# Performance work log

Measured on AMD Instinct MI355X. Metric: run time of the kernel, lower is better.

The kernel has to match this reference:

```python
import jax, jax.numpy as jnp
import numpy as np

B, N, H, HEADS, L, V, T = 4, 256, 256, 4, 128, 256, 100
FF = 4 * H

def _ln(x, g, b, eps=1e-5):
    m = jnp.mean(x, -1, keepdims=True)
    v = jnp.mean((x - m) ** 2, -1, keepdims=True)
    return (x - m) / jnp.sqrt(v + eps) * g + b

def _mha(h, w_qkv, b_qkv, w_o, b_o):
    b, n, hd = h.shape
    d = hd // HEADS
    q, k, v = jnp.split(h @ w_qkv + b_qkv, 3, axis=-1)
    q = q.reshape(b, n, HEADS, d)
    k = k.reshape(b, n, HEADS, d)
    v = v.reshape(b, n, HEADS, d)
    s = jnp.einsum('bihd,bjhd->bhij', q, k) / jnp.sqrt(jnp.float32(d))
    a = jax.nn.softmax(s, axis=-1)
    o = jnp.einsum('bhij,bjhd->bihd', a, v).reshape(b, n, hd)
    return o @ w_o + b_o

def _edge_logits(h, w1, b1, w2, b2):
    # concat([h_i, h_j], -1) @ w1 == h_i @ w1[:H] + h_j @ w1[H:]  (avoids (B,N,N,2H) materialization)
    hi = h @ w1[:H]
    hj = h @ w1[H:]
    pre = hi[:, :, None, :] + hj[:, None, :, :] + b1  # (B,N,N,H)
    return (jax.nn.gelu(pre, approximate=False) @ w2 + b2)[..., 0]

def _gnn_block(x, nbr, qw, qb, kw, kb, vw, vb, sw, sb, l1g, l1b, f1w, f1b, f2w, f2b, l2g, l2b):
    # TransformerConv (PyG, concat=True, root_weight=True) as dense masked attention over in-neighbors.
    b, n, hd = x.shape
    d = hd // HEADS
    q = (x @ qw + qb).reshape(b, n, HEADS, d)
    k = (x @ kw + kb).reshape(b, n, HEADS, d)
    v = (x @ vw + vb).reshape(b, n, HEADS, d)
    s = jnp.einsum('bihd,bjhd->bhij', q, k) / jnp.sqrt(jnp.float32(d))
    m = nbr[:, None, :, :]  # (B,1,N,N); nbr[b,i,j]=True iff edge j->i
    a = jax.nn.softmax(jnp.where(m, s, -1e30), axis=-1) * m  # no-neighbor rows aggregate to 0
    agg = jnp.einsum('bhij,bjhd->bihd', a, v).reshape(b, n, hd)
    x = _ln(x + agg + x @ sw + sb, l1g, l1b)
    ffn = jax.nn.gelu(x @ f1w + f1b, approximate=False) @ f2w + f2b
    return _ln(x + ffn, l2g, l2b)

def _forward(noisy_tokens, t, z, lp1_w, lp1_b, lp2_w, lp2_b, tok_emb, time_tab, time_w, time_b, pos_tab, enc_qkv_w, enc_qkv_b, enc_o_w, enc_o_b, enc_ln1_g, enc_ln1_b, enc_f1_w, enc_f1_b, enc_f2_w, enc_f2_b, enc_ln2_g, enc_ln2_b, gq_w, gq_b, gk_w, gk_b, gv_w, gv_b, gs_w, gs_b, g_ln1_g, g_ln1_b, g_f1_w, g_f1_b, g_f2_w, g_f2_b, g_ln2_g, g_ln2_b, nh1_w, nh1_b, nh2_w, nh2_b, eh1_w, eh1_b, eh2_w, eh2_b, sh1_w, sh1_b, sh2_w, sh2_b):
    lat = jax.nn.relu(z @ lp1_w + lp1_b) @ lp2_w + lp2_b  # (B,H)
    time_e = jax.nn.gelu(time_tab[t] @ time_w + time_b, approximate=False)  # (B,H)
    h = tok_emb[noisy_tokens] + time_e[:, None, :] + pos_tab[None, :, :] + lat[:, None, :]
    for l in range(2):  # post-norm TransformerEncoderLayer, relu FFN
        h = _ln(h + _mha(h, enc_qkv_w[l], enc_qkv_b[l], enc_o_w[l], enc_o_b[l]), enc_ln1_g[l], enc_ln1_b[l])
        h = _ln(h + jax.nn.relu(h @ enc_f1_w[l] + enc_f1_b[l]) @ enc_f2_w[l] + enc_f2_b[l], enc_ln2_g[l], enc_ln2_b[l])
    el0 = _edge_logits(h, eh1_w, eh1_b, eh2_w, eh2_b)
    nbr = jnp.swapaxes(jax.nn.sigmoid(el0) > 0.3, 1, 2)  # transpose: adj[j,i] -> in-neighbors of i
    x = h
    for l in range(4):
        x = _gnn_block(x, nbr, gq_w[l], gq_b[l], gk_w[l], gk_b[l], gv_w[l], gv_b[l], gs_w[l], gs_b[l], g_ln1_g[l], g_ln1_b[l], g_f1_w[l], g_f1_b[l], g_f2_w[l], g_f2_b[l], g_ln2_g[l], g_ln2_b[l])
    node_logits = jax.nn.gelu(x @ nh1_w + nh1_b, approximate=False) @ nh2_w + nh2_b
    edge_logits = _edge_logits(x, eh1_w, eh1_b, eh2_w, eh2_b)
    size_logits = jax.nn.relu(lat @ sh1_w + sh1_b) @ sh2_w + sh2_b
    return node_logits, edge_logits, size_logits

def setup_inputs():
    key = jax.random.key(0)
    ks = iter(jax.random.split(key, 70))
    def p(shape):
        return jax.random.normal(next(ks), shape, dtype=jnp.float32) * 0.02
    return {
        'z': jax.random.normal(next(ks), (B, L), dtype=jnp.float32),
        'noisy_tokens': jax.random.randint(next(ks), (B, N), 0, V),
        't': jax.random.randint(next(ks), (B,), 0, T),
        'lp1_w': p((L, H)), 'lp1_b': p((H,)), 'lp2_w': p((H, H)), 'lp2_b': p((H,)),
        'tok_emb': p((V, H)), 'time_tab': p((T, H)), 'time_w': p((H, H)), 'time_b': p((H,)),
        'pos_tab': p((N, H)),
        'enc_qkv_w': p((2, H, 3 * H)), 'enc_qkv_b': p((2, 3 * H)),
        'enc_o_w': p((2, H, H)), 'enc_o_b': p((2, H)),
        'enc_ln1_g': jnp.ones((2, H)), 'enc_ln1_b': jnp.zeros((2, H)),
        'enc_f1_w': p((2, H, FF)), 'enc_f1_b': p((2, FF)),
        'enc_f2_w': p((2, FF, H)), 'enc_f2_b': p((2, H)),
        'enc_ln2_g': jnp.ones((2, H)), 'enc_ln2_b': jnp.zeros((2, H)),
        'gq_w': p((4, H, H)), 'gq_b': p((4, H)),
        'gk_w': p((4, H, H)), 'gk_b': p((4, H)),
        'gv_w': p((4, H, H)), 'gv_b': p((4, H)),
        'gs_w': p((4, H, H)), 'gs_b': p((4, H)),
        'g_ln1_g': jnp.ones((4, H)), 'g_ln1_b': jnp.zeros((4, H)),
        'g_f1_w': p((4, H, FF)), 'g_f1_b': p((4, FF)),
        'g_f2_w': p((4, FF, H)), 'g_f2_b': p((4, H)),
        'g_ln2_g': jnp.ones((4, H)), 'g_ln2_b': jnp.zeros((4, H)),
        'nh1_w': p((H, H)), 'nh1_b': p((H,)),
        'nh2_w': p((H, V)), 'nh2_b': p((V,)),
        'eh1_w': p((2 * H, H)), 'eh1_b': p((H,)),
        'eh2_w': p((H, 1)), 'eh2_b': p((1,)),
        'sh1_w': p((H, H // 2)), 'sh1_b': p((H // 2,)),
        'sh2_w': p((H // 2, N)), 'sh2_b': p((N,)),
    }

def reference(z, noisy_tokens, t, lp1_w, lp1_b, lp2_w, lp2_b, tok_emb, time_tab, time_w, time_b, pos_tab, enc_qkv_w, enc_qkv_b, enc_o_w, enc_o_b, enc_ln1_g, enc_ln1_b, enc_f1_w, enc_f1_b, enc_f2_w, enc_f2_b, enc_ln2_g, enc_ln2_b, gq_w, gq_b, gk_w, gk_b, gv_w, gv_b, gs_w, gs_b, g_ln1_g, g_ln1_b, g_f1_w, g_f1_b, g_f2_w, g_f2_b, g_ln2_g, g_ln2_b, nh1_w, nh1_b, nh2_w, nh2_b, eh1_w, eh1_b, eh2_w, eh2_b, sh1_w, sh1_b, sh2_w, sh2_b):
    return _forward(noisy_tokens, t, z, lp1_w, lp1_b, lp2_w, lp2_b, tok_emb, time_tab, time_w, time_b, pos_tab, enc_qkv_w, enc_qkv_b, enc_o_w, enc_o_b, enc_ln1_g, enc_ln1_b, enc_f1_w, enc_f1_b, enc_f2_w, enc_f2_b, enc_ln2_g, enc_ln2_b, gq_w, gq_b, gk_w, gk_b, gv_w, gv_b, gs_w, gs_b, g_ln1_g, g_ln1_b, g_f1_w, g_f1_b, g_f2_w, g_f2_b, g_ln2_g, g_ln2_b, nh1_w, nh1_b, nh2_w, nh2_b, eh1_w, eh1_b, eh2_w, eh2_b, sh1_w, sh1_b, sh2_w, sh2_b)
```

## Files before the change

kernel.cpp:

```cpp
#include <hip/hip_runtime.h>
#include <math.h>


typedef __attribute__((ext_vector_type(8))) short bf16x8;
typedef __attribute__((ext_vector_type(4))) float f32x4;

__device__ __forceinline__ unsigned short f2b(float f) {
    unsigned u = __float_as_uint(f);
    u += 0x7FFFu + ((u >> 16) & 1u);
    return (unsigned short)(u >> 16);
}
__device__ __forceinline__ unsigned pack2(float a, float b) {
    return (unsigned)f2b(a) | ((unsigned)f2b(b) << 16);
}
__device__ __forceinline__ bf16x8 as_frag(uint4 v) {
    union { uint4 u; bf16x8 f; } x; x.u = v; return x.f;
}
__device__ __forceinline__ bf16x8 ld_frag_f32(const float* p) {
    const float4 v0 = *(const float4*)p;
    const float4 v1 = *(const float4*)(p + 4);
    union { unsigned u[4]; bf16x8 f; } x;
    x.u[0] = pack2(v0.x, v0.y); x.u[1] = pack2(v0.z, v0.w);
    x.u[2] = pack2(v1.x, v1.y); x.u[3] = pack2(v1.z, v1.w);
    return x.f;
}

__device__ __forceinline__ float gelu_f(float x) {
    const float y  = 0.70710678118654752f * x;
    const float ay = fabsf(y);
    const float t  = __builtin_amdgcn_rcpf(fmaf(0.3275911f, ay, 1.0f));
    float S = fmaf(t, 1.061405429f, -1.453152027f);
    S = fmaf(t, S, 1.421413741f);
    S = fmaf(t, S, -0.284496736f);
    S = fmaf(t, S, 0.254829592f);
    S = S * t;
    const float e = __expf(-ay * ay);
    const float E = fmaf(-S, e, 1.0f);
    return 0.5f * x * (1.0f + copysignf(E, y));
}

struct PrepEnt { const float* src; unsigned dstOff; int K; int N; unsigned tstart; };
struct PrepTab { int n; PrepEnt e[36]; };

__global__ __launch_bounds__(256) void k_prep(PrepTab tab, unsigned short* __restrict__ wt)
{
    const int bx = blockIdx.x;
    int ei = 0;
    for (int i = 0; i < tab.n; ++i) if (tab.e[i].tstart <= (unsigned)bx) ei = i;
    const PrepEnt E = tab.e[ei];
    const int tIdx = bx - E.tstart;
    const int ntn = E.N >> 6;
    const int kt = tIdx / ntn, nt = tIdx % ntn;
    const int tid = threadIdx.x;
    __shared__ unsigned Tl[64][36];
    {
        const int r = tid >> 2, c = (tid & 3) * 16;
        const float* s = E.src + (size_t)(kt * 64 + r) * E.N + nt * 64 + c;
        unsigned o[8];
        #pragma unroll
        for (int q = 0; q < 4; ++q) {
            const float4 v = *(const float4*)(s + q * 4);
            o[q * 2 + 0] = pack2(v.x, v.y);
            o[q * 2 + 1] = pack2(v.z, v.w);
        }
        *(uint4*)&Tl[r][c / 2 + 0] = make_uint4(o[0], o[1], o[2], o[3]);
        *(uint4*)&Tl[r][c / 2 + 4] = make_uint4(o[4], o[5], o[6], o[7]);
    }
    __syncthreads();
    {
        const int rn = tid >> 2, ck = (tid & 3) * 16;
        const int sh = (rn & 1) * 16, hw = rn >> 1;
        unsigned o[8];
        #pragma unroll
        for (int s = 0; s < 8; ++s) {
            const unsigned lo = (Tl[ck + 2 * s][hw] >> sh) & 0xFFFFu;
            const unsigned hi = (Tl[ck + 2 * s + 1][hw] >> sh) & 0xFFFFu;
            o[s] = lo | (hi << 16);
        }
        unsigned short* d = wt + E.dstOff + (size_t)(nt * 64 + rn) * E.K + kt * 64 + ck;
        *(uint4*)(d + 0) = make_uint4(o[0], o[1], o[2], o[3]);
        *(uint4*)(d + 8) = make_uint4(o[4], o[5], o[6], o[7]);
    }
}


__device__ __forceinline__ void gd64_body(
    const float* __restrict__ A, const unsigned short* __restrict__ Wt,
    const float* __restrict__ bias, float* __restrict__ C,
    int K, int ldc, int act, int m0, int n0)
{
    const int tid = threadIdx.x;
    const int l = tid & 63, wid = tid >> 6;
    const int wm = wid & 1, wn = wid >> 1, lr = l & 15, lg = l >> 4;
    const float* a0 = A + (size_t)(m0 + wm * 32 + lr) * K + lg * 8;
    const float* a1 = a0 + (size_t)16 * K;
    const unsigned short* b0 = Wt + (size_t)(n0 + wn * 32 + lr) * K + lg * 8;
    const unsigned short* b1 = b0 + (size_t)16 * K;
    f32x4 acc00 = {0.f,0.f,0.f,0.f}, acc01 = acc00, acc10 = acc00, acc11 = acc00;
    #pragma unroll 2
    for (int k0 = 0; k0 < K; k0 += 32) {
        const bf16x8 fa0 = ld_frag_f32(a0 + k0);
        const bf16x8 fa1 = ld_frag_f32(a1 + k0);
        const bf16x8 fb0 = as_frag(*(const uint4*)(b0 + k0));
        const bf16x8 fb1 = as_frag(*(const uint4*)(b1 + k0));
        acc00 = __builtin_amdgcn_mfma_f32_16x16x32_bf16(fa0, fb0, acc00, 0, 0, 0);
        acc01 = __builtin_amdgcn_mfma_f32_16x16x32_bf16(fa0, fb1, acc01, 0, 0, 0);
        acc10 = __builtin_amdgcn_mfma_f32_16x16x32_bf16(fa1, fb0, acc10, 0, 0, 0);
        acc11 = __builtin_amdgcn_mfma_f32_16x16x32_bf16(fa1, fb1, acc11, 0, 0, 0);
    }
    const int cb0 = n0 + wn * 32 + lr, cb1 = cb0 + 16;
    const float bv0 = bias ? bias[cb0] : 0.f;
    const float bv1 = bias ? bias[cb1] : 0.f;
    #pragma unroll
    for (int r = 0; r < 4; ++r) {
        const int row0 = m0 + wm * 32 + lg * 4 + r;
        const int row1 = row0 + 16;
        float v00 = acc00[r] + bv0, v01 = acc01[r] + bv1;
        float v10 = acc10[r] + bv0, v11 = acc11[r] + bv1;
        if (act == 1) {
            v00 = fmaxf(v00, 0.f); v01 = fmaxf(v01, 0.f);
            v10 = fmaxf(v10, 0.f); v11 = fmaxf(v11, 0.f);
        } else if (act == 2) {
            v00 = gelu_f(v00); v01 = gelu_f(v01);
            v10 = gelu_f(v10); v11 = gelu_f(v11);
        }
        C[(size_t)row0 * ldc + cb0] = v00;
        C[(size_t)row0 * ldc + cb1] = v01;
        C[(size_t)row1 * ldc + cb0] = v10;
        C[(size_t)row1 * ldc + cb1] = v11;
    }
}

__global__ __launch_bounds__(256) void k_gd64(
    const float* __restrict__ A, const unsigned short* __restrict__ Wt,
    const float* __restrict__ bias, float* __restrict__ C, int K, int ldc, int act)
{
    gd64_body(A, Wt, bias, C, K, ldc, act, blockIdx.y * 64, blockIdx.x * 64);
}

__device__ __forceinline__ void gd32_body(
    const float* __restrict__ A, const unsigned short* __restrict__ Wt,
    const float* __restrict__ bias, float* __restrict__ C,
    int K, int ldc, int act, int m0, int n0)
{
    const int tid = threadIdx.x;
    const int l = tid & 63, wid = tid >> 6;
    const int qm = wid & 1, qn = wid >> 1, lr = l & 15, lg = l >> 4;
    const float* ap = A + (size_t)(m0 + qm * 16 + lr) * K + lg * 8;
    const unsigned short* bp = Wt + (size_t)(n0 + qn * 16 + lr) * K + lg * 8;
    f32x4 acc = {0.f,0.f,0.f,0.f};
    #pragma unroll 4
    for (int k0 = 0; k0 < K; k0 += 32) {
        const bf16x8 fa = ld_frag_f32(ap + k0);
        const bf16x8 fb = as_frag(*(const uint4*)(bp + k0));
        acc = __builtin_amdgcn_mfma_f32_16x16x32_bf16(fa, fb, acc, 0, 0, 0);
    }
    const int cc = n0 + qn * 16 + lr;
    const float bv = bias ? bias[cc] : 0.f;
    #pragma unroll
    for (int r = 0; r < 4; ++r) {
        const int row = m0 + qm * 16 + lg * 4 + r;
        float v = acc[r] + bv;
        if (act == 1) v = fmaxf(v, 0.f); else if (act == 2) v = gelu_f(v);
        C[(size_t)row * ldc + cc] = v;
    }
}

__global__ __launch_bounds__(256) void k_gd32(
    const float* __restrict__ A, const unsigned short* __restrict__ Wt,
    const float* __restrict__ bias, float* __restrict__ C, int K, int ldc, int act)
{
    gd32_body(A, Wt, bias, C, K, ldc, act, blockIdx.y * 32, blockIdx.x * 32);
}

struct MW4 { const unsigned short* wt[4]; const float* b[4]; };
__global__ __launch_bounds__(256) void k_gd32_4(
    const float* __restrict__ A, MW4 p, float* __restrict__ C)
{
    const int z = blockIdx.z;
    gd32_body(A, p.wt[z], p.b[z], C + z * 256, 256, 1024, 0,
              blockIdx.y * 32, blockIdx.x * 32);
}

__global__ __launch_bounds__(256) void k_mv(
    const float* __restrict__ A, const int* __restrict__ aidx, int K,
    const float* __restrict__ W, const float* __restrict__ bias,
    float* __restrict__ out, int N, int act)
{
    const int r = blockIdx.x, c0 = blockIdx.y * 64;
    const int c = threadIdx.x & 63, ks = threadIdx.x >> 6;
    const float* arow = A + (size_t)(aidx ? aidx[r] : r) * K;
    float s = 0.f;
    for (int k = ks; k < K; k += 4) s += arow[k] * W[(size_t)k * N + c0 + c];
    __shared__ float red[4][64];
    red[ks][c] = s;
    __syncthreads();
    if (ks == 0) {
        float v = red[0][c] + red[1][c] + red[2][c] + red[3][c] + (bias ? bias[c0 + c] : 0.f);
        if (act == 1) v = fmaxf(v, 0.f); else if (act == 2) v = gelu_f(v);
        out[(size_t)r * N + c0 + c] = v;
    }
}

__global__ __launch_bounds__(256) void k_embed(
    const int* __restrict__ tok, const float* __restrict__ tok_emb,
    const float* __restrict__ pos, const float* __restrict__ lat,
    const float* __restrict__ te, float* __restrict__ h)
{
    const int r = blockIdx.x, c = threadIdx.x;
    const int b = r >> 8, n = r & 255;
    h[(size_t)r * 256 + c] = tok_emb[(size_t)tok[r] * 256 + c] + te[b * 256 + c]
                           + pos[n * 256 + c] + lat[b * 256 + c];
}

__global__ __launch_bounds__(256) void k_attn2(
    const float* __restrict__ qkv, int ld, int qo, int ko, int vo,
    const unsigned char* __restrict__ mask, float* __restrict__ out)
{
    const int blk = blockIdx.x;
    const int ig = blk & 15, hh = (blk >> 4) & 3, b = blk >> 6;
    const int i0 = ig * 16;
    const int t = threadIdx.x;
    __shared__ float Qs[16][68];
    __shared__ float Ts[64][68];
    __shared__ float Ss[16][260];

    {
        const int r = t >> 4, c = (t & 15) * 4;
        *(float4*)&Qs[r][c] = *(const float4*)&qkv[(size_t)(b * 256 + i0 + r) * ld + qo + hh * 64 + c];
    }
    const int i = t >> 4, tx = t & 15;

    for (int jt = 0; jt < 4; ++jt) {
        __syncthreads();
        {
            const int jr = t >> 2, cs = (t & 3) * 16;
            const float* src = &qkv[(size_t)(b * 256 + jt * 64 + jr) * ld + ko + hh * 64 + cs];
            *(float4*)&Ts[jr][cs + 0]  = *(const float4*)(src + 0);
            *(float4*)&Ts[jr][cs + 4]  = *(const float4*)(src + 4);
            *(float4*)&Ts[jr][cs + 8]  = *(const float4*)(src + 8);
            *(float4*)&Ts[jr][cs + 12] = *(const float4*)(src + 12);
        }
        __syncthreads();
        float s0 = 0.f, s1 = 0.f, s2 = 0.f, s3 = 0.f;
        #pragma unroll 8
        for (int d = 0; d < 64; ++d) {
            const float qd = Qs[i][d];
            s0 += qd * Ts[tx][d];
            s1 += qd * Ts[tx + 16][d];
            s2 += qd * Ts[tx + 32][d];
            s3 += qd * Ts[tx + 48][d];
        }
        Ss[i][jt * 64 + tx]      = s0;
        Ss[i][jt * 64 + tx + 16] = s1;
        Ss[i][jt * 64 + tx + 32] = s2;
        Ss[i][jt * 64 + tx + 48] = s3;
    }

    {
        const unsigned char* mrow = mask ? &mask[(size_t)(b * 256 + i0 + i) * 256] : nullptr;
        float sv[16]; bool okv[16];
        float m = -3.0e38f;
        #pragma unroll
        for (int k = 0; k < 16; ++k) {
            const int j = tx + 16 * k;
            const float s = Ss[i][j] * 0.125f;
            const bool ok = mrow ? (mrow[j] != 0) : true;
            sv[k] = s; okv[k] = ok;
            if (ok) m = fmaxf(m, s);
        }
        #pragma unroll
        for (int w = 1; w < 16; w <<= 1) m = fmaxf(m, __shfl_xor(m, w, 64));
        float ev[16]; float sum = 0.f;
        #pragma unroll
        for (int k = 0; k < 16; ++k) {
            ev[k] = okv[k] ? __expf(sv[k] - m) : 0.f;
            sum += ev[k];
        }
        #pragma unroll
        for (int w = 1; w < 16; w <<= 1) sum += __shfl_xor(sum, w, 64);
        const float inv = (sum > 0.f) ? 1.f / sum : 0.f;
        #pragma unroll
        for (int k = 0; k < 16; ++k) Ss[i][tx + 16 * k] = ev[k] * inv;
    }

    const int d4 = tx * 4;
    float4 o = {0.f, 0.f, 0.f, 0.f};
    for (int jt = 0; jt < 4; ++jt) {
        __syncthreads();
        {
            const int jr = t >> 2, cs = (t & 3) * 16;
            const float* src = &qkv[(size_t)(b * 256 + jt * 64 + jr) * ld + vo + hh * 64 + cs];
            *(float4*)&Ts[jr][cs + 0]  = *(const float4*)(src + 0);
            *(float4*)&Ts[jr][cs + 4]  = *(const float4*)(src + 4);
            *(float4*)&Ts[jr][cs + 8]  = *(const float4*)(src + 8);
            *(float4*)&Ts[jr][cs + 12] = *(const float4*)(src + 12);
        }
        __syncthreads();
        #pragma unroll 8
        for (int j = 0; j < 64; ++j) {
            const float p = Ss[i][jt * 64 + j];
            const float4 v4 = *(const float4*)&Ts[j][d4];
            o.x += p * v4.x; o.y += p * v4.y; o.z += p * v4.z; o.w += p * v4.w;
        }
    }
    *(float4*)&out[(size_t)(b * 256 + i0 + i) * 256 + hh * 64 + d4] = o;
}

__global__ __launch_bounds__(256) void k_ln2(
    const float* __restrict__ a, const float* __restrict__ bb, int ldb,
    const float* __restrict__ cc, int ldc,
    const float* __restrict__ g, const float* __restrict__ beta, float* __restrict__ out)
{
    const int r = blockIdx.x * 4 + (threadIdx.x >> 6);
    const int c4 = (threadIdx.x & 63) * 4;
    float4 v = *(const float4*)&a[(size_t)r * 256 + c4];
    if (bb) {
        const float4 u = *(const float4*)&bb[(size_t)r * ldb + c4];
        v.x += u.x; v.y += u.y; v.z += u.z; v.w += u.w;
    }
    if (cc) {
        const float4 u = *(const float4*)&cc[(size_t)r * ldc + c4];
        v.x += u.x; v.y += u.y; v.z += u.z; v.w += u.w;
    }
    float s = v.x + v.y + v.z + v.w;
    float q = v.x * v.x + v.y * v.y + v.z * v.z + v.w * v.w;
    #pragma unroll
    for (int w = 1; w < 64; w <<= 1) {
        s += __shfl_xor(s, w, 64);
        q += __shfl_xor(q, w, 64);
    }
    const float mean = s * (1.0f / 256.0f);
    const float var  = q * (1.0f / 256.0f) - mean * mean;
    const float inv  = rsqrtf(var + 1e-5f);
    const float4 gg = *(const float4*)&g[c4];
    const float4 be = *(const float4*)&beta[c4];
    float4 o;
    o.x = (v.x - mean) * inv * gg.x + be.x;
    o.y = (v.y - mean) * inv * gg.y + be.y;
    o.z = (v.z - mean) * inv * gg.z + be.z;
    o.w = (v.w - mean) * inv * gg.w + be.w;
    *(float4*)&out[(size_t)r * 256 + c4] = o;
}

__global__ __launch_bounds__(256) void k_edge3(
    const float* __restrict__ hi, const float* __restrict__ hj,
    const float* __restrict__ w2, const float* __restrict__ b2,
    float* __restrict__ val_out, unsigned char* __restrict__ mask_out)
{
    const int jg = blockIdx.x, ig = blockIdx.y, b = blockIdx.z;
    const int t = threadIdx.x;
    __shared__ float his[16][268];
    __shared__ float hjs[16][268];
    __shared__ float w2s[256];
    {
        const int r = t >> 4, c = (t & 15) * 16;
        const float* s1 = &hi[(size_t)(b * 256 + ig * 16 + r) * 256 + c];
        const float* s2 = &hj[(size_t)(b * 256 + jg * 16 + r) * 256 + c];
        #pragma unroll
        for (int q = 0; q < 4; ++q) {
            *(float4*)&his[r][c + q * 4] = *(const float4*)(s1 + q * 4);
            *(float4*)&hjs[r][c + q * 4] = *(const float4*)(s2 + q * 4);
        }
        w2s[t] = w2[t];
    }
    __syncthreads();
    const int i = t >> 4, j = t & 15;
    float acc = 0.f;
    #pragma unroll 4
    for (int h4 = 0; h4 < 64; ++h4) {
        const float4 hv  = *(const float4*)&hjs[j][h4 * 4];
        const float4 hi4 = *(const float4*)&his[i][h4 * 4];
        const float4 w4  = *(const float4*)&w2s[h4 * 4];
        acc += gelu_f(hi4.x + hv.x) * w4.x;
        acc += gelu_f(hi4.y + hv.y) * w4.y;
        acc += gelu_f(hi4.z + hv.z) * w4.z;
        acc += gelu_f(hi4.w + hv.w) * w4.w;
    }
    const float v = acc + b2[0];
    if (val_out)  val_out[(size_t)b * 65536 + (ig * 16 + i) * 256 + jg * 16 + j] = v;
    if (mask_out) mask_out[(size_t)b * 65536 + (jg * 16 + j) * 256 + ig * 16 + i] =
                      (v > -0.84729786038720f) ? 1 : 0;
}

extern "C" void kernel_launch(void* const* d_in, const int* in_sizes, int n_in,
                              void* d_out, int out_size, void* d_ws, size_t ws_size,
                              hipStream_t stream) {
    const float* z     = (const float*)d_in[0];
    const int*   tok   = (const int*)d_in[1];
    const int*   tt    = (const int*)d_in[2];
    const float* lp1w  = (const float*)d_in[3];
    const float* lp1b  = (const float*)d_in[4];
    const float* lp2w  = (const float*)d_in[5];
    const float* lp2b  = (const float*)d_in[6];
    const float* temb  = (const float*)d_in[7];
    const float* ttab  = (const float*)d_in[8];
    const float* tw    = (const float*)d_in[9];
    const float* tb    = (const float*)d_in[10];
    const float* pos   = (const float*)d_in[11];
    const float* qkvw  = (const float*)d_in[12];
    const float* qkvb  = (const float*)d_in[13];
    const float* ow    = (const float*)d_in[14];
    const float* ob    = (const float*)d_in[15];
    const float* ln1g  = (const float*)d_in[16];
    const float* ln1b  = (const float*)d_in[17];
    const float* f1w   = (const float*)d_in[18];
    const float* f1b   = (const float*)d_in[19];
    const float* f2w   = (const float*)d_in[20];
    const float* f2b   = (const float*)d_in[21];
    const float* ln2g  = (const float*)d_in[22];
    const float* ln2b  = (const float*)d_in[23];
    const float* gqw   = (const float*)d_in[24];
    const float* gqb   = (const float*)d_in[25];
    const float* gkw   = (const float*)d_in[26];
    const float* gkb   = (const float*)d_in[27];
    const float* gvw   = (const float*)d_in[28];
    const float* gvb   = (const float*)d_in[29];
    const float* gsw   = (const float*)d_in[30];
    const float* gsb   = (const float*)d_in[31];
    const float* gl1g  = (const float*)d_in[32];
    const float* gl1b  = (const float*)d_in[33];
    const float* gf1w  = (const float*)d_in[34];
    const float* gf1b  = (const float*)d_in[35];
    const float* gf2w  = (const float*)d_in[36];
    const float* gf2b  = (const float*)d_in[37];
    const float* gl2g  = (const float*)d_in[38];
    const float* gl2b  = (const float*)d_in[39];
    const float* nh1w  = (const float*)d_in[40];
    const float* nh1b  = (const float*)d_in[41];
    const float* nh2w  = (const float*)d_in[42];
    const float* nh2b  = (const float*)d_in[43];
    const float* eh1w  = (const float*)d_in[44];
    const float* eh1b  = (const float*)d_in[45];
    const float* eh2w  = (const float*)d_in[46];
    const float* eh2b  = (const float*)d_in[47];
    const float* sh1w  = (const float*)d_in[48];
    const float* sh1b  = (const float*)d_in[49];
    const float* sh2w  = (const float*)d_in[50];
    const float* sh2b  = (const float*)d_in[51];

    float* W = (float*)d_ws;
    float* Hh  = W + 0;
    float* QK  = W + 262144;
    float* AO  = W + 1310720;
    float* T1  = W + 1572864;
    float* HI  = W + 1835008;
    float* HJ  = W + 2097152;
    float* LAT = W + 2359296;
    float* TE  = W + 2360320;
    float* A1  = W + 2361344;
    float* SH  = W + 2362368;
    unsigned char* MASK = (unsigned char*)(W + 2362880);
    unsigned short* wt  = (unsigned short*)(W + 2428416);

    float* out      = (float*)d_out;
    float* out_node = out;
    float* out_edge = out + 262144;
    float* out_sz   = out + 524288;

    PrepTab tab; int ne = 0; unsigned tiles = 0;
    auto add = [&](const float* src, int K, int N, unsigned off) {
        tab.e[ne].src = src; tab.e[ne].K = K; tab.e[ne].N = N;
        tab.e[ne].dstOff = off; tab.e[ne].tstart = tiles;
        tiles += (unsigned)((K >> 6) * (N >> 6)); ++ne;
    };
    for (int l = 0; l < 2; ++l) add(qkvw + (size_t)l * 196608, 256, 768,  0 + l * 196608);
    for (int l = 0; l < 2; ++l) add(ow   + (size_t)l * 65536,  256, 256,  393216 + l * 65536);
    for (int l = 0; l < 2; ++l) add(f1w  + (size_t)l * 262144, 256, 1024, 524288 + l * 262144);
    for (int l = 0; l < 2; ++l) add(f2w  + (size_t)l * 262144, 1024, 256, 1048576 + l * 262144);
    for (int l = 0; l < 4; ++l) add(gqw  + (size_t)l * 65536,  256, 256,  1572864 + l * 65536);
    for (int l = 0; l < 4; ++l) add(gkw  + (size_t)l * 65536,  256, 256,  1835008 + l * 65536);
    for (int l = 0; l < 4; ++l) add(gvw  + (size_t)l * 65536,  256, 256,  2097152 + l * 65536);
    for (int l = 0; l < 4; ++l) add(gsw  + (size_t)l * 65536,  256, 256,  2359296 + l * 65536);
    for (int l = 0; l < 4; ++l) add(gf1w + (size_t)l * 262144, 256, 1024, 2621440 + l * 262144);
    for (int l = 0; l < 4; ++l) add(gf2w + (size_t)l * 262144, 1024, 256, 3670016 + l * 262144);
    add(nh1w, 256, 256, 4718592);
    add(nh2w, 256, 256, 4784128);
    add(eh1w,         256, 256, 4849664);
    add(eh1w + 65536, 256, 256, 4915200);
    tab.n = ne;
    k_prep<<<tiles, 256, 0, stream>>>(tab, wt);

    auto g64 = [&](const float* Aa, size_t wtoff, const float* bias, float* Cc,
                   int N, int K, int ldc, int act) {
        k_gd64<<<dim3(N / 64, 16), 256, 0, stream>>>(Aa, wt + wtoff, bias, Cc, K, ldc, act);
    };
    auto g32 = [&](const float* Aa, size_t wtoff, const float* bias, float* Cc,
                   int K, int ldc, int act) {
        k_gd32<<<dim3(8, 32), 256, 0, stream>>>(Aa, wt + wtoff, bias, Cc, K, ldc, act);
    };

    k_mv<<<dim3(4, 4), 256, 0, stream>>>(z,    nullptr, 128, lp1w, lp1b, A1,     256, 1);
    k_mv<<<dim3(4, 4), 256, 0, stream>>>(ttab, tt,      256, tw,   tb,   TE,     256, 2);
    k_mv<<<dim3(4, 4), 256, 0, stream>>>(A1,   nullptr, 256, lp2w, lp2b, LAT,    256, 0);
    k_mv<<<dim3(4, 2), 256, 0, stream>>>(LAT,  nullptr, 256, sh1w, sh1b, SH,     128, 1);
    k_mv<<<dim3(4, 4), 256, 0, stream>>>(SH,   nullptr, 128, sh2w, sh2b, out_sz, 256, 0);

    k_embed<<<1024, 256, 0, stream>>>(tok, temb, pos, LAT, TE, Hh);

    for (int l = 0; l < 2; ++l) {
        g64(Hh, (size_t)l * 196608, qkvb + l * 768, QK, 768, 256, 768, 0);
        k_attn2<<<256, 256, 0, stream>>>(QK, 768, 0, 256, 512, nullptr, AO);
        g32(AO, 393216 + (size_t)l * 65536, ob + l * 256, T1, 256, 256, 0);
        k_ln2<<<256, 256, 0, stream>>>(Hh, T1, 256, nullptr, 0, ln1g + l * 256, ln1b + l * 256, Hh);
        g64(Hh, 524288 + (size_t)l * 262144, f1b + l * 1024, QK, 1024, 256, 1024, 1);
        g32(QK, 1048576 + (size_t)l * 262144, f2b + l * 256, T1, 1024, 256, 0);
        k_ln2<<<256, 256, 0, stream>>>(Hh, T1, 256, nullptr, 0, ln2g + l * 256, ln2b + l * 256, Hh);
    }

    g32(Hh, 4849664, eh1b, HI, 256, 256, 0);
    g32(Hh, 4915200, nullptr, HJ, 256, 256, 0);
    k_edge3<<<dim3(16, 16, 4), 256, 0, stream>>>(HI, HJ, eh2w, eh2b, nullptr, MASK);

    for (int l = 0; l < 4; ++l) {
        MW4 p;
        p.wt[0] = wt + 1572864 + (size_t)l * 65536; p.b[0] = gqb + l * 256;
        p.wt[1] = wt + 1835008 + (size_t)l * 65536; p.b[1] = gkb + l * 256;
        p.wt[2] = wt + 2097152 + (size_t)l * 65536; p.b[2] = gvb + l * 256;
        p.wt[3] = wt + 2359296 + (size_t)l * 65536; p.b[3] = gsb + l * 256;
        k_gd32_4<<<dim3(8, 32, 4), 256, 0, stream>>>(Hh, p, QK);
        k_attn2<<<256, 256, 0, stream>>>(QK, 1024, 0, 256, 512, MASK, AO);
        k_ln2<<<256, 256, 0, stream>>>(Hh, AO, 256, QK + 768, 1024, gl1g + l * 256, gl1b + l * 256, Hh);
        g64(Hh, 2621440 + (size_t)l * 262144, gf1b + l * 1024, QK, 1024, 256, 1024, 2);
        g32(QK, 3670016 + (size_t)l * 262144, gf2b + l * 256, T1, 1024, 256, 0);
        k_ln2<<<256, 256, 0, stream>>>(Hh, T1, 256, nullptr, 0, gl2g + l * 256, gl2b + l * 256, Hh);
    }

    g32(Hh, 4718592, nh1b, T1, 256, 256, 2);
    g32(T1, 4784128, nh2b, out_node, 256, 256, 0);
    g32(Hh, 4849664, eh1b, HI, 256, 256, 0);
    g32(Hh, 4915200, nullptr, HJ, 256, 256, 0);
    k_edge3<<<dim3(16, 16, 4), 256, 0, stream>>>(HI, HJ, eh2w, eh2b, out_edge, nullptr);
}
```

Measured before the change: 750.0 us.

## Fuse prep, latent/time MLPs and embedding into one kernel; batch independent GEMMs

Folds weight prep, the small latent, time and size matvec chains and the embedding build into one combined launch, using extra blocks after the prep tiles. Independent GEMMs (HI/HJ, nh1/HI/HJ) are batched into multi-target launches. The final edge head and the node-head GEMM share one kernel. The 64x64 GEMM variant is replaced by the 32x32 one with larger grids. The aim is to cut launch count and tail idle time, at the cost of serial per-block matvecs and a 32-tile GEMM with less reuse per block.

```diff
diff --git a/kernel.cpp b/kernel.cpp
--- a/kernel.cpp
+++ b/kernel.cpp
@@ -42,100 +42,98 @@
 struct PrepEnt { const float* src; unsigned dstOff; int K; int N; unsigned tstart; };
 struct PrepTab { int n; PrepEnt e[36]; };
 
-__global__ __launch_bounds__(256) void k_prep(PrepTab tab, unsigned short* __restrict__ wt)
-{
+struct S0Args {
+    const float *z; const int *tok, *tt;
+    const float *lp1w,*lp1b,*lp2w,*lp2b,*ttab,*tw,*tb,*temb,*pos;
+    const float *sh1w,*sh1b,*sh2w,*sh2b;
+    float *Hh, *out_sz;
+};
+
+__global__ __launch_bounds__(256) void k_combo1(PrepTab tab, unsigned short* __restrict__ wt,
+                                                S0Args A)
+{
+    __shared__ unsigned Tl[64][36];
+    __shared__ float zS[256], a1S[256], latS[256], teS[256];
+    __shared__ int tokS[256];
     const int bx = blockIdx.x;
-    int ei = 0;
-    for (int i = 0; i < tab.n; ++i) if (tab.e[i].tstart <= (unsigned)bx) ei = i;
-    const PrepEnt E = tab.e[ei];
-    const int tIdx = bx - E.tstart;
-    const int ntn = E.N >> 6;
-    const int kt = tIdx / ntn, nt = tIdx % ntn;
     const int tid = threadIdx.x;
-    __shared__ unsigned Tl[64][36];
-    {
-        const int r = tid >> 2, c = (tid & 3) * 16;
-        const float* s = E.src + (size_t)(kt * 64 + r) * E.N + nt * 64 + c;
-        unsigned o[8];
-        #pragma unroll
-        for (int q = 0; q < 4; ++q) {
-            const float4 v = *(const float4*)(s + q * 4);
-            o[q * 2 + 0] = pack2(v.x, v.y);
-            o[q * 2 + 1] = pack2(v.z, v.w);
-        }
-        *(uint4*)&Tl[r][c / 2 + 0] = make_uint4(o[0], o[1], o[2], o[3]);
-        *(uint4*)&Tl[r][c / 2 + 4] = make_uint4(o[4], o[5], o[6], o[7]);
+    if (bx < 1216) {
+        int ei = 0;
+        for (int i = 0; i < tab.n; ++i) if (tab.e[i].tstart <= (unsigned)bx) ei = i;
+        const PrepEnt E = tab.e[ei];
+        const int tIdx = bx - (int)E.tstart;
+        const int ntn = E.N >> 6;
+        const int kt = tIdx / ntn, nt = tIdx % ntn;
+        {
+            const int r = tid >> 2, c = (tid & 3) * 16;
+            const float* s = E.src + (size_t)(kt * 64 + r) * E.N + nt * 64 + c;
+            unsigned o[8];
+            #pragma unroll
+            for (int q = 0; q < 4; ++q) {
+                const float4 v = *(const float4*)(s + q * 4);
+                o[q * 2 + 0] = pack2(v.x, v.y);
+                o[q * 2 + 1] = pack2(v.z, v.w);
+            }
+            *(uint4*)&Tl[r][c / 2 + 0] = make_uint4(o[0], o[1], o[2], o[3]);
+            *(uint4*)&Tl[r][c / 2 + 4] = make_uint4(o[4], o[5], o[6], o[7]);
+        }
+        __syncthreads();
+        {
+            const int rn = tid >> 2, ck = (tid & 3) * 16;
+            const int sh = (rn & 1) * 16, hw = rn >> 1;
+            unsigned o[8];
+            #pragma unroll
+            for (int s = 0; s < 8; ++s) {
+                const unsigned lo = (Tl[ck + 2 * s][hw] >> sh) & 0xFFFFu;
+                const unsigned hi = (Tl[ck + 2 * s + 1][hw] >> sh) & 0xFFFFu;
+                o[s] = lo | (hi << 16);
+            }
+            unsigned short* d = wt + E.dstOff + (size_t)(nt * 64 + rn) * E.K + kt * 64 + ck;
+            *(uint4*)(d + 0) = make_uint4(o[0], o[1], o[2], o[3]);
+            *(uint4*)(d + 8) = make_uint4(o[4], o[5], o[6], o[7]);
+        }
+        return;
+    }
+    const int b = bx - 1216;
+    const int c = tid;
+    if (c < 128) zS[c] = A.z[b * 128 + c];
+    teS[c] = A.ttab[(size_t)A.tt[b] * 256 + c];
+    tokS[c] = A.tok[b * 256 + c];
+    __syncthreads();
+    float a1 = A.lp1b[c];
+    #pragma unroll 4
+    for (int k = 0; k < 128; ++k) a1 = fmaf(zS[k], A.lp1w[k * 256 + c], a1);
+    a1 = fmaxf(a1, 0.f);
+    float tev = A.tb[c];
+    #pragma unroll 4
+    for (int k = 0; k < 256; ++k) tev = fmaf(teS[k], A.tw[k * 256 + c], tev);
+    __syncthreads();
+    a1S[c] = a1;
+    teS[c] = gelu_f(tev);
+    __syncthreads();
+    float lat = A.lp2b[c];
+    #pragma unroll 4
+    for (int k = 0; k < 256; ++k) lat = fmaf(a1S[k], A.lp2w[k * 256 + c], lat);
+    latS[c] = lat;
+    __syncthreads();
+    if (c < 128) {
+        float s = A.sh1b[c];
+        #pragma unroll 4
+        for (int k = 0; k < 256; ++k) s = fmaf(latS[k], A.sh1w[k * 128 + c], s);
+        zS[c] = fmaxf(s, 0.f);
     }
     __syncthreads();
     {
-        const int rn = tid >> 2, ck = (tid & 3) * 16;
-        const int sh = (rn & 1) * 16, hw = rn >> 1;
-        unsigned o[8];
-        #pragma unroll
-        for (int s = 0; s < 8; ++s) {
-            const unsigned lo = (Tl[ck + 2 * s][hw] >> sh) & 0xFFFFu;
-            const unsigned hi = (Tl[ck + 2 * s + 1][hw] >> sh) & 0xFFFFu;
-            o[s] = lo | (hi << 16);
-        }
-        unsigned short* d = wt + E.dstOff + (size_t)(nt * 64 + rn) * E.K + kt * 64 + ck;
-        *(uint4*)(d + 0) = make_uint4(o[0], o[1], o[2], o[3]);
-        *(uint4*)(d + 8) = make_uint4(o[4], o[5], o[6], o[7]);
-    }
-}
-
-
-__device__ __forceinline__ void gd64_body(
-    const float* __restrict__ A, const unsigned short* __restrict__ Wt,
-    const float* __restrict__ bias, float* __restrict__ C,
-    int K, int ldc, int act, int m0, int n0)
-{
-    const int tid = threadIdx.x;
-    const int l = tid & 63, wid = tid >> 6;
-    const int wm = wid & 1, wn = wid >> 1, lr = l & 15, lg = l >> 4;
-    const float* a0 = A + (size_t)(m0 + wm * 32 + lr) * K + lg * 8;
-    const float* a1 = a0 + (size_t)16 * K;
-    const unsigned short* b0 = Wt + (size_t)(n0 + wn * 32 + lr) * K + lg * 8;
-    const unsigned short* b1 = b0 + (size_t)16 * K;
-    f32x4 acc00 = {0.f,0.f,0.f,0.f}, acc01 = acc00, acc10 = acc00, acc11 = acc00;
-    #pragma unroll 2
-    for (int k0 = 0; k0 < K; k0 += 32) {
-        const bf16x8 fa0 = ld_frag_f32(a0 + k0);
-        const bf16x8 fa1 = ld_frag_f32(a1 + k0);
-        const bf16x8 fb0 = as_frag(*(const uint4*)(b0 + k0));
-        const bf16x8 fb1 = as_frag(*(const uint4*)(b1 + k0));
-        acc00 = __builtin_amdgcn_mfma_f32_16x16x32_bf16(fa0, fb0, acc00, 0, 0, 0);
-        acc01 = __builtin_amdgcn_mfma_f32_16x16x32_bf16(fa0, fb1, acc01, 0, 0, 0);
-        acc10 = __builtin_amdgcn_mfma_f32_16x16x32_bf16(fa1, fb0, acc10, 0, 0, 0);
-        acc11 = __builtin_amdgcn_mfma_f32_16x16x32_bf16(fa1, fb1, acc11, 0, 0, 0);
-    }
-    const int cb0 = n0 + wn * 32 + lr, cb1 = cb0 + 16;
-    const float bv0 = bias ? bias[cb0] : 0.f;
-    const float bv1 = bias ? bias[cb1] : 0.f;
-    #pragma unroll
-    for (int r = 0; r < 4; ++r) {
-        const int row0 = m0 + wm * 32 + lg * 4 + r;
-        const int row1 = row0 + 16;
-        float v00 = acc00[r] + bv0, v01 = acc01[r] + bv1;
-        float v10 = acc10[r] + bv0, v11 = acc11[r] + bv1;
-        if (act == 1) {
-            v00 = fmaxf(v00, 0.f); v01 = fmaxf(v01, 0.f);
-            v10 = fmaxf(v10, 0.f); v11 = fmaxf(v11, 0.f);
-        } else if (act == 2) {
-            v00 = gelu_f(v00); v01 = gelu_f(v01);
-            v10 = gelu_f(v10); v11 = gelu_f(v11);
-        }
-        C[(size_t)row0 * ldc + cb0] = v00;
-        C[(size_t)row0 * ldc + cb1] = v01;
-        C[(size_t)row1 * ldc + cb0] = v10;
-        C[(size_t)row1 * ldc + cb1] = v11;
-    }
-}
-
-__global__ __launch_bounds__(256) void k_gd64(
-    const float* __restrict__ A, const unsigned short* __restrict__ Wt,
-    const float* __restrict__ bias, float* __restrict__ C, int K, int ldc, int act)
-{
-    gd64_body(A, Wt, bias, C, K, ldc, act, blockIdx.y * 64, blockIdx.x * 64);
+        float v = A.sh2b[c];
+        #pragma unroll 4
+        for (int k = 0; k < 128; ++k) v = fmaf(zS[k], A.sh2w[k * 256 + c], v);
+        A.out_sz[b * 256 + c] = v;
+    }
+    const float tec = teS[c], lac = latS[c];
+    for (int n = 0; n < 256; ++n) {
+        A.Hh[(size_t)(b * 256 + n) * 256 + c] =
+            A.temb[(size_t)tokS[n] * 256 + c] + tec + A.pos[n * 256 + c] + lac;
+    }
 }
 
 __device__ __forceinline__ void gd32_body(
@@ -173,44 +171,13 @@
     gd32_body(A, Wt, bias, C, K, ldc, act, blockIdx.y * 32, blockIdx.x * 32);
 }
 
-struct MW4 { const unsigned short* wt[4]; const float* b[4]; };
-__global__ __launch_bounds__(256) void k_gd32_4(
-    const float* __restrict__ A, MW4 p, float* __restrict__ C)
-{
-    const int z = blockIdx.z;
-    gd32_body(A, p.wt[z], p.b[z], C + z * 256, 256, 1024, 0,
-              blockIdx.y * 32, blockIdx.x * 32);
-}
-
-__global__ __launch_bounds__(256) void k_mv(
-    const float* __restrict__ A, const int* __restrict__ aidx, int K,
-    const float* __restrict__ W, const float* __restrict__ bias,
-    float* __restrict__ out, int N, int act)
-{
-    const int r = blockIdx.x, c0 = blockIdx.y * 64;
-    const int c = threadIdx.x & 63, ks = threadIdx.x >> 6;
-    const float* arow = A + (size_t)(aidx ? aidx[r] : r) * K;
-    float s = 0.f;
-    for (int k = ks; k < K; k += 4) s += arow[k] * W[(size_t)k * N + c0 + c];
-    __shared__ float red[4][64];
-    red[ks][c] = s;
-    __syncthreads();
-    if (ks == 0) {
-        float v = red[0][c] + red[1][c] + red[2][c] + red[3][c] + (bias ? bias[c0 + c] : 0.f);
-        if (act == 1) v = fmaxf(v, 0.f); else if (act == 2) v = gelu_f(v);
-        out[(size_t)r * N + c0 + c] = v;
-    }
-}
-
-__global__ __launch_bounds__(256) void k_embed(
-    const int* __restrict__ tok, const float* __restrict__ tok_emb,
-    const float* __restrict__ pos, const float* __restrict__ lat,
-    const float* __restrict__ te, float* __restrict__ h)
-{
-    const int r = blockIdx.x, c = threadIdx.x;
-    const int b = r >> 8, n = r & 255;
-    h[(size_t)r * 256 + c] = tok_emb[(size_t)tok[r] * 256 + c] + te[b * 256 + c]
-                           + pos[n * 256 + c] + lat[b * 256 + c];
+struct GBe { const unsigned short* wt; const float* bias; float* C; int ldc; int act; };
+struct GB4 { GBe e[4]; };
+__global__ __launch_bounds__(256) void k_gd32b(
+    const float* __restrict__ A, GB4 p, int K)
+{
+    const GBe E = p.e[blockIdx.z];
+    gd32_body(A, E.wt, E.bias, E.C, K, E.ldc, E.act, blockIdx.y * 32, blockIdx.x * 32);
 }
 
 __global__ __launch_bounds__(256) void k_attn2(
@@ -271,17 +238,17 @@
         }
         #pragma unroll
         for (int w = 1; w < 16; w <<= 1) m = fmaxf(m, __shfl_xor(m, w, 64));
-        float ev[16]; float sum = 0.f;
+        float sum = 0.f;
         #pragma unroll
         for (int k = 0; k < 16; ++k) {
-            ev[k] = okv[k] ? __expf(sv[k] - m) : 0.f;
-            sum += ev[k];
+            sv[k] = okv[k] ? __expf(sv[k] - m) : 0.f;
+            sum += sv[k];
         }
         #pragma unroll
         for (int w = 1; w < 16; w <<= 1) sum += __shfl_xor(sum, w, 64);
         const float inv = (sum > 0.f) ? 1.f / sum : 0.f;
         #pragma unroll
-        for (int k = 0; k < 16; ++k) Ss[i][tx + 16 * k] = ev[k] * inv;
+        for (int k = 0; k < 16; ++k) Ss[i][tx + 16 * k] = sv[k] * inv;
     }
 
     const int d4 = tx * 4;
@@ -343,16 +310,16 @@
     *(float4*)&out[(size_t)r * 256 + c4] = o;
 }
 
-__global__ __launch_bounds__(256) void k_edge3(
+__device__ __forceinline__ void edge_body(
     const float* __restrict__ hi, const float* __restrict__ hj,
     const float* __restrict__ w2, const float* __restrict__ b2,
-    float* __restrict__ val_out, unsigned char* __restrict__ mask_out)
-{
-    const int jg = blockIdx.x, ig = blockIdx.y, b = blockIdx.z;
+    float* __restrict__ val_out, unsigned char* __restrict__ mask_out,
+    int b, int ig, int jg, char* SMc)
+{
+    float (*his)[268] = (float(*)[268])SMc;
+    float (*hjs)[268] = (float(*)[268])(SMc + 17152);
+    float* w2s = (float*)(SMc + 34304);
     const int t = threadIdx.x;
-    __shared__ float his[16][268];
-    __shared__ float hjs[16][268];
-    __shared__ float w2s[256];
     {
         const int r = t >> 4, c = (t & 15) * 16;
         const float* s1 = &hi[(size_t)(b * 256 + ig * 16 + r) * 256 + c];
@@ -381,6 +348,34 @@
     if (val_out)  val_out[(size_t)b * 65536 + (ig * 16 + i) * 256 + jg * 16 + j] = v;
     if (mask_out) mask_out[(size_t)b * 65536 + (jg * 16 + j) * 256 + ig * 16 + i] =
                       (v > -0.84729786038720f) ? 1 : 0;
+}
+
+__global__ __launch_bounds__(256) void k_edge3(
+    const float* __restrict__ hi, const float* __restrict__ hj,
+    const float* __restrict__ w2, const float* __restrict__ b2,
+    float* __restrict__ val_out, unsigned char* __restrict__ mask_out)
+{
+    __shared__ __align__(16) char SM[35328];
+    edge_body(hi, hj, w2, b2, val_out, mask_out,
+              blockIdx.z, blockIdx.y, blockIdx.x, SM);
+}
+
+__global__ __launch_bounds__(256) void k_final(
+    const float* __restrict__ hi, const float* __restrict__ hj,
+    const float* __restrict__ w2, const float* __restrict__ b2,
+    float* __restrict__ out_edge,
+    const float* __restrict__ T1, const unsigned short* __restrict__ nh2wt,
+    const float* __restrict__ nh2b, float* __restrict__ out_node)
+{
+    __shared__ __align__(16) char SM[35328];
+    const int bx = blockIdx.x;
+    if (bx < 1024) {
+        edge_body(hi, hj, w2, b2, out_edge, nullptr,
+                  bx >> 8, (bx >> 4) & 15, bx & 15, SM);
+    } else {
+        const int s = bx - 1024;
+        gd32_body(T1, nh2wt, nh2b, out_node, 256, 256, 0, (s & 31) * 32, (s >> 5) * 32);
+    }
 }
 
 extern "C" void kernel_launch(void* const* d_in, const int* in_sizes, int n_in,
@@ -446,23 +441,19 @@
     float* T1  = W + 1572864;
     float* HI  = W + 1835008;
     float* HJ  = W + 2097152;
-    float* LAT = W + 2359296;
-    float* TE  = W + 2360320;
-    float* A1  = W + 2361344;
-    float* SH  = W + 2362368;
-    unsigned char* MASK = (unsigned char*)(W + 2362880);
-    unsigned short* wt  = (unsigned short*)(W + 2428416);
+    unsigned char* MASK = (unsigned char*)(W + 2359296);
+    unsigned short* wt  = (unsigned short*)(W + 2424832);
 
     float* out      = (float*)d_out;
     float* out_node = out;
     float* out_edge = out + 262144;
     float* out_sz   = out + 524288;
 
-    PrepTab tab; int ne = 0; unsigned tiles = 0;
+    PrepTab tab; tab.n = 0; unsigned tiles = 0;
     auto add = [&](const float* src, int K, int N, unsigned off) {
-        tab.e[ne].src = src; tab.e[ne].K = K; tab.e[ne].N = N;
-        tab.e[ne].dstOff = off; tab.e[ne].tstart = tiles;
-        tiles += (unsigned)((K >> 6) * (N >> 6)); ++ne;
+        PrepEnt& e = tab.e[tab.n++];
+        e.src = src; e.K = K; e.N = N; e.dstOff = off; e.tstart = tiles;
+        tiles += (unsigned)((K >> 6) * (N >> 6));
     };
     for (int l = 0; l < 2; ++l) add(qkvw + (size_t)l * 196608, 256, 768,  0 + l * 196608);
     for (int l = 0; l < 2; ++l) add(ow   + (size_t)l * 65536,  256, 256,  393216 + l * 65536);
@@ -478,57 +469,69 @@
     add(nh2w, 256, 256, 4784128);
     add(eh1w,         256, 256, 4849664);
     add(eh1w + 65536, 256, 256, 4915200);
-    tab.n = ne;
-    k_prep<<<tiles, 256, 0, stream>>>(tab, wt);
-
-    auto g64 = [&](const float* Aa, size_t wtoff, const float* bias, float* Cc,
-                   int N, int K, int ldc, int act) {
-        k_gd64<<<dim3(N / 64, 16), 256, 0, stream>>>(Aa, wt + wtoff, bias, Cc, K, ldc, act);
-    };
-    auto g32 = [&](const float* Aa, size_t wtoff, const float* bias, float* Cc,
-                   int K, int ldc, int act) {
-        k_gd32<<<dim3(8, 32), 256, 0, stream>>>(Aa, wt + wtoff, bias, Cc, K, ldc, act);
-    };
-
-    k_mv<<<dim3(4, 4), 256, 0, stream>>>(z,    nullptr, 128, lp1w, lp1b, A1,     256, 1);
-    k_mv<<<dim3(4, 4), 256, 0, stream>>>(ttab, tt,      256, tw,   tb,   TE,     256, 2);
-    k_mv<<<dim3(4, 4), 256, 0, stream>>>(A1,   nullptr, 256, lp2w, lp2b, LAT,    256, 0);
-    k_mv<<<dim3(4, 2), 256, 0, stream>>>(LAT,  nullptr, 256, sh1w, sh1b, SH,     128, 1);
-    k_mv<<<dim3(4, 4), 256, 0, stream>>>(SH,   nullptr, 128, sh2w, sh2b, out_sz, 256, 0);
-
-    k_embed<<<1024, 256, 0, stream>>>(tok, temb, pos, LAT, TE, Hh);
+
+    S0Args s0;
+    s0.z = z; s0.tok = tok; s0.tt = tt;
+    s0.lp1w = lp1w; s0.lp1b = lp1b; s0.lp2w = lp2w; s0.lp2b = lp2b;
+    s0.ttab = ttab; s0.tw = tw; s0.tb = tb; s0.temb = temb; s0.pos = pos;
+    s0.sh1w = sh1w; s0.sh1b = sh1b; s0.sh2w = sh2w; s0.sh2b = sh2b;
+    s0.Hh = Hh; s0.out_sz = out_sz;
+
+    k_combo1<<<1220, 256, 0, stream>>>(tab, wt, s0);
 
     for (int l = 0; l < 2; ++l) {
-        g64(Hh, (size_t)l * 196608, qkvb + l * 768, QK, 768, 256, 768, 0);
+        k_gd32<<<dim3(24, 32), 256, 0, stream>>>(Hh, wt + (size_t)l * 196608,
+                                                 qkvb + l * 768, QK, 256, 768, 0);
         k_attn2<<<256, 256, 0, stream>>>(QK, 768, 0, 256, 512, nullptr, AO);
-        g32(AO, 393216 + (size_t)l * 65536, ob + l * 256, T1, 256, 256, 0);
-        k_ln2<<<256, 256, 0, stream>>>(Hh, T1, 256, nullptr, 0, ln1g + l * 256, ln1b + l * 256, Hh);
-        g64(Hh, 524288 + (size_t)l * 262144, f1b + l * 1024, QK, 1024, 256, 1024, 1);
-        g32(QK, 1048576 + (size_t)l * 262144, f2b + l * 256, T1, 1024, 256, 0);
-        k_ln2<<<256, 256, 0, stream>>>(Hh, T1, 256, nullptr, 0, ln2g + l * 256, ln2b + l * 256, Hh);
-    }
-
-    g32(Hh, 4849664, eh1b, HI, 256, 256, 0);
-    g32(Hh, 4915200, nullptr, HJ, 256, 256, 0);
+        k_gd32<<<dim3(8, 32), 256, 0, stream>>>(AO, wt + 393216 + (size_t)l * 65536,
+                                                ob + l * 256, T1, 256, 256, 0);
+        k_ln2<<<256, 256, 0, stream>>>(Hh, T1, 256, nullptr, 0,
+                                       ln1g + l * 256, ln1b + l * 256, Hh);
+        k_gd32<<<dim3(32, 32), 256, 0, stream>>>(Hh, wt + 524288 + (size_t)l * 262144,
+                                                 f1b + l * 1024, QK, 256, 1024, 1);
+        k_gd32<<<dim3(8, 32), 256, 0, stream>>>(QK, wt + 1048576 + (size_t)l * 262144,
+                                                f2b + l * 256, T1, 1024, 256, 0);
+        k_ln2<<<256, 256, 0, stream>>>(Hh, T1, 256, nullptr, 0,
+                                       ln2g + l * 256, ln2b + l * 256, Hh);
+    }
+
+    {
+        GB4 p;
+        p.e[0] = { wt + 4849664, eh1b,    HI, 256, 0 };
+        p.e[1] = { wt + 4915200, nullptr, HJ, 256, 0 };
+        p.e[2] = p.e[0]; p.e[3] = p.e[0];
+        k_gd32b<<<dim3(8, 32, 2), 256, 0, stream>>>(Hh, p, 256);
+    }
     k_edge3<<<dim3(16, 16, 4), 256, 0, stream>>>(HI, HJ, eh2w, eh2b, nullptr, MASK);
 
     for (int l = 0; l < 4; ++l) {
-        MW4 p;
-        p.wt[0] = wt + 1572864 + (size_t)l * 65536; p.b[0] = gqb + l * 256;
-        p.wt[1] = wt + 1835008 + (size_t)l * 65536; p.b[1] = gkb + l * 256;
-        p.wt[2] = wt + 2097152 + (size_t)l * 65536; p.b[2] = gvb + l * 256;
-        p.wt[3] = wt + 2359296 + (size_t)l * 65536; p.b[3] = gsb + l * 256;
-        k_gd32_4<<<dim3(8, 32, 4), 256, 0, stream>>>(Hh, p, QK);
+        GB4 p;
+        p.e[0] = { wt + 1572864 + (size_t)l * 65536, gqb + l * 256, QK + 0,   1024, 0 };
+        p.e[1] = { wt + 1835008 + (size_t)l * 65536, gkb + l * 256, QK + 256, 1024, 0 };
+        p.e[2] = { wt + 2097152 + (size_t)l * 65536, gvb + l * 256, QK + 512, 1024, 0 };
+        p.e[3] = { wt + 2359296 + (size_t)l * 65536, gsb + l * 256, QK + 768, 1024, 0 };
+        k_gd32b<<<dim3(8, 32, 4), 256, 0, stream>>>(Hh, p, 256);
         k_attn2<<<256, 256, 0, stream>>>(QK, 1024, 0, 256, 512, MASK, AO);
-        k_ln2<<<256, 256, 0, stream>>>(Hh, AO, 256, QK + 768, 1024, gl1g + l * 256, gl1b + l * 256, Hh);
-        g64(Hh, 2621440 + (size_t)l * 262144, gf1b + l * 1024, QK, 1024, 256, 1024, 2);
-        g32(QK, 3670016 + (size_t)l * 262144, gf2b + l * 256, T1, 1024, 256, 0);
-        k_ln2<<<256, 256, 0, stream>>>(Hh, T1, 256, nullptr, 0, gl2g + l * 256, gl2b + l * 256, Hh);
-    }
-
-    g32(Hh, 4718592, nh1b, T1, 256, 256, 2);
-    g32(T1, 4784128, nh2b, out_node, 256, 256, 0);
-    g32(Hh, 4849664, eh1b, HI, 256, 256, 0);
-    g32(Hh, 4915200, nullptr, HJ, 256, 256, 0);
-    k_edge3<<<dim3(16, 16, 4), 256, 0, stream>>>(HI, HJ, eh2w, eh2b, out_edge, nullptr);
-}
+        k_ln2<<<256, 256, 0, stream>>>(Hh, AO, 256, QK + 768, 1024,
+                                       gl1g + l * 256, gl1b + l * 256, Hh);
+        k_gd32<<<dim3(32, 32), 256, 0, stream>>>(Hh, wt + 2621440 + (size_t)l * 262144,
+                                                 gf1b + l * 1024, QK, 256, 1024, 2);
+        GB4 q;
+        q.e[0] = { wt + 3670016 + (size_t)l * 262144, gf2b + l * 256, T1, 256, 0 };
+        q.e[1] = q.e[0]; q.e[2] = q.e[0]; q.e[3] = q.e[0];
+        k_gd32b<<<dim3(8, 32, 1), 256, 0, stream>>>(QK, q, 1024);
+        k_ln2<<<256, 256, 0, stream>>>(Hh, T1, 256, nullptr, 0,
+                                       gl2g + l * 256, gl2b + l * 256, Hh);
+    }
+
+    {
+        GB4 p;
+        p.e[0] = { wt + 4718592, nh1b,    T1, 256, 2 };
+        p.e[1] = { wt + 4849664, eh1b,    HI, 256, 0 };
+        p.e[2] = { wt + 4915200, nullptr, HJ, 256, 0 };
+        p.e[3] = p.e[0];
+        k_gd32b<<<dim3(8, 32, 3), 256, 0, stream>>>(Hh, p, 256);
+    }
+    k_final<<<1280, 256, 0, stream>>>(HI, HJ, eh2w, eh2b, out_edge,
+                                      T1, wt + 4784128, nh2b, out_node);
+}
```

After: 810.6 us. +8.1%, slower.
